# Performance work log

Measured on AMD Instinct MI355X. Metric: run time of the kernel, lower is better.

The kernel has to match this reference:

```python
import jax, jax.numpy as jnp
import numpy as np

N_NODES = 100000
N_EDGES = 6400000


def setup_inputs() -> dict:
    key = jax.random.key(0)
    k1, k2, k3 = jax.random.split(key, 3)
    x = jax.random.normal(k1, (N_NODES, 1), dtype=jnp.float32)
    edge_index = jax.random.randint(k2, (2, N_EDGES), 0, N_NODES, dtype=jnp.int64)
    edge_weight = jax.random.normal(k3, (N_EDGES,), dtype=jnp.float32)
    return {"x": x, "edge_index": edge_index, "edge_weight": edge_weight}


def reference(x, edge_index, edge_weight):
    # flow='target_to_source': messages come from x[edge_index[1]] and are
    # scatter-added into nodes edge_index[0].
    src = edge_index[0]  # aggregation target (flow reversed)
    dst = edge_index[1]  # message source
    msgs = edge_weight[:, None] * x[dst]  # [E, 1]
    out = jax.ops.segment_sum(msgs, src, num_segments=N_NODES)  # [N, 1]
    return out
```

## Files before the change

### kernel.cpp

```cpp
#include <hip/hip_runtime.h>

#define N_NODES 100000
#define N_EDGES 6400000
#define RANGES 4
#define RANGE_S 25000
#define NB 64
#define BLK 1024
#define FIX_SCALE 1048576.0f
#define FIX_INV   (1.0f / 1048576.0f)

#define TBLOCKS 256
#define TTHREADS 1024
#define EPB (N_EDGES / TBLOCKS)
#define GPB (EPB / 8)
#define LDSN 80000

__global__ void zero_out_kernel(float* __restrict__ out, int n) {
    int i = blockIdx.x * blockDim.x + threadIdx.x;
    if (i < n) out[i] = 0.0f;
}

__global__ void __launch_bounds__(256) scatter_direct_kernel(
        const float* __restrict__ x, const int* __restrict__ ei,
        const float* __restrict__ w, float* __restrict__ out) {
    int t = blockIdx.x * blockDim.x + threadIdx.x;
    int e0 = t * 4;
    if (e0 >= N_EDGES) return;
    int4   s4 = *reinterpret_cast<const int4*>(ei + e0);
    int4   d4 = *reinterpret_cast<const int4*>(ei + N_EDGES + e0);
    float4 w4 = *reinterpret_cast<const float4*>(w + e0);
    atomicAdd(&out[s4.x], w4.x * x[d4.x]);
    atomicAdd(&out[s4.y], w4.y * x[d4.y]);
    atomicAdd(&out[s4.z], w4.z * x[d4.z]);
    atomicAdd(&out[s4.w], w4.w * x[d4.w]);
}

__device__ __forceinline__ unsigned bf16_rne(float f) {
    unsigned b = __float_as_uint(f);
    b += 0x7FFFu + ((b >> 16) & 1u);
    return b >> 16;
}
__device__ __forceinline__ float bf16_to_f(unsigned h) {
    return __uint_as_float(h << 16);
}

__global__ void __launch_bounds__(TTHREADS, 4) transform_kernel(
        const float* __restrict__ x, const int* __restrict__ ei,
        const float* __restrict__ w, unsigned short* __restrict__ msg) {
    __shared__ unsigned short xh[LDSN];
    const int tid  = threadIdx.x;
    const int base = blockIdx.x * EPB;
    const int* dstp = ei + N_EDGES;

    const float4* xs = reinterpret_cast<const float4*>(x);
    for (int j = tid; j < LDSN / 8; j += TTHREADS) {
        float4 f0 = xs[j * 2], f1 = xs[j * 2 + 1];
        uint4 pk;
        pk.x = bf16_rne(f0.x) | (bf16_rne(f0.y) << 16);
        pk.y = bf16_rne(f0.z) | (bf16_rne(f0.w) << 16);
        pk.z = bf16_rne(f1.x) | (bf16_rne(f1.y) << 16);
        pk.w = bf16_rne(f1.z) | (bf16_rne(f1.w) << 16);
        *reinterpret_cast<uint4*>(&xh[j * 8]) = pk;
    }
    __syncthreads();

    #pragma unroll
    for (int k = 0; k < 4; ++k) {
        int idx = k * TTHREADS + tid;
        if (idx < GPB) {
            int e0 = base + idx * 8;
            int4   da = *reinterpret_cast<const int4*>(dstp + e0);
            int4   db = *reinterpret_cast<const int4*>(dstp + e0 + 4);
            float4 wa = *reinterpret_cast<const float4*>(w + e0);
            float4 wb = *reinterpret_cast<const float4*>(w + e0 + 4);

            unsigned a0 = (unsigned)da.x, a1 = (unsigned)da.y,
                     a2 = (unsigned)da.z, a3 = (unsigned)da.w,
                     a4 = (unsigned)db.x, a5 = (unsigned)db.y,
                     a6 = (unsigned)db.z, a7 = (unsigned)db.w;
            float v0 = bf16_to_f(xh[a0 < LDSN ? a0 : 0u]);
            float v1 = bf16_to_f(xh[a1 < LDSN ? a1 : 0u]);
            float v2 = bf16_to_f(xh[a2 < LDSN ? a2 : 0u]);
            float v3 = bf16_to_f(xh[a3 < LDSN ? a3 : 0u]);
            float v4 = bf16_to_f(xh[a4 < LDSN ? a4 : 0u]);
            float v5 = bf16_to_f(xh[a5 < LDSN ? a5 : 0u]);
            float v6 = bf16_to_f(xh[a6 < LDSN ? a6 : 0u]);
            float v7 = bf16_to_f(xh[a7 < LDSN ? a7 : 0u]);
            if (a0 >= LDSN) v0 = x[a0];
            if (a1 >= LDSN) v1 = x[a1];
            if (a2 >= LDSN) v2 = x[a2];
            if (a3 >= LDSN) v3 = x[a3];
            if (a4 >= LDSN) v4 = x[a4];
            if (a5 >= LDSN) v5 = x[a5];
            if (a6 >= LDSN) v6 = x[a6];
            if (a7 >= LDSN) v7 = x[a7];

            uint4 o;
            o.x = bf16_rne(wa.x * v0) | (bf16_rne(wa.y * v1) << 16);
            o.y = bf16_rne(wa.z * v2) | (bf16_rne(wa.w * v3) << 16);
            o.z = bf16_rne(wb.x * v4) | (bf16_rne(wb.y * v5) << 16);
            o.w = bf16_rne(wb.z * v6) | (bf16_rne(wb.w * v7) << 16);
            *reinterpret_cast<uint4*>(msg + e0) = o;
        }
    }
}

__global__ void __launch_bounds__(BLK) bin_kernel(
        const int* __restrict__ ei, const unsigned short* __restrict__ msg,
        unsigned short* __restrict__ partial) {
    __shared__ int bins[RANGE_S];
    const int b    = blockIdx.x;
    const int xcd  = b & 7;
    const int slot = b >> 3;
    const int r    = slot & 3;
    const int c    = (slot >> 2) * 8 + xcd;

    for (int i = threadIdx.x; i < RANGE_S; i += BLK) bins[i] = 0;
    __syncthreads();

    const int chunk = N_EDGES / NB;
    const int base  = c * chunk;
    const int end   = base + chunk;
    const int lo    = r * RANGE_S;

    for (int e = base + (int)threadIdx.x * 8; e < end; e += BLK * 8) {
        int4 sa = *reinterpret_cast<const int4*>(ei + e);
        int4 sb = *reinterpret_cast<const int4*>(ei + e + 4);
        uint4 mm = *reinterpret_cast<const uint4*>(msg + e);

        unsigned a[8] = {(unsigned)(sa.x-lo),(unsigned)(sa.y-lo),(unsigned)(sa.z-lo),(unsigned)(sa.w-lo),
                         (unsigned)(sb.x-lo),(unsigned)(sb.y-lo),(unsigned)(sb.z-lo),(unsigned)(sb.w-lo)};
        float f[8] = {
            __uint_as_float((mm.x & 0xFFFFu) << 16), __uint_as_float(mm.x & 0xFFFF0000u),
            __uint_as_float((mm.y & 0xFFFFu) << 16), __uint_as_float(mm.y & 0xFFFF0000u),
            __uint_as_float((mm.z & 0xFFFFu) << 16), __uint_as_float(mm.z & 0xFFFF0000u),
            __uint_as_float((mm.w & 0xFFFFu) << 16), __uint_as_float(mm.w & 0xFFFF0000u)
        };
        int mi[8];
        #pragma unroll
        for (int k = 0; k < 8; ++k) mi[k] = (int)__builtin_rintf(f[k] * FIX_SCALE);
        #pragma unroll
        for (int k = 0; k < 8; ++k) {
            if (a[k] < RANGE_S) atomicAdd(&bins[a[k]], mi[k]);
        }
    }
    __syncthreads();

    unsigned short* outp = partial + (size_t)(r * NB + c) * RANGE_S;
    for (int i = threadIdx.x; i < RANGE_S / 4; i += BLK) {
        int4 v = *reinterpret_cast<const int4*>(&bins[i * 4]);
        uint2 pk;
        pk.x = bf16_rne((float)v.x * FIX_INV) | (bf16_rne((float)v.y * FIX_INV) << 16);
        pk.y = bf16_rne((float)v.z * FIX_INV) | (bf16_rne((float)v.w * FIX_INV) << 16);
        *reinterpret_cast<uint2*>(outp + i * 4) = pk;
    }
}

__global__ void reduce_range_kernel(const unsigned short* __restrict__ partial,
                                    float* __restrict__ out) {
    int i = blockIdx.x * blockDim.x + threadIdx.x;
    int n0 = i * 4;
    if (n0 >= N_NODES) return;
    int r = n0 / RANGE_S;
    int s = n0 - r * RANGE_S;
    const unsigned short* bp = partial + (size_t)(r * NB) * RANGE_S + s;
    float4 acc = make_float4(0.f, 0.f, 0.f, 0.f);
    for (int j = 0; j < NB; ++j) {
        uint2 v = *reinterpret_cast<const uint2*>(bp + (size_t)j * RANGE_S);
        acc.x += bf16_to_f(v.x & 0xFFFFu);
        acc.y += bf16_to_f(v.x >> 16);
        acc.z += bf16_to_f(v.y & 0xFFFFu);
        acc.w += bf16_to_f(v.y >> 16);
    }
    *reinterpret_cast<float4*>(out + n0) = acc;
}

extern "C" void kernel_launch(void* const* d_in, const int* in_sizes, int n_in,
                              void* d_out, int out_size, void* d_ws, size_t ws_size,
                              hipStream_t stream) {
    const float* x   = (const float*)d_in[0];
    const int*   ei  = (const int*)d_in[1];
    const float* w   = (const float*)d_in[2];
    float*       out = (float*)d_out;

    const size_t msg_bytes     = (size_t)N_EDGES * 2;
    const size_t partial_bytes = (size_t)RANGES * NB * RANGE_S * 2;

    if (ws_size >= msg_bytes + partial_bytes) {
        unsigned short* msg     = (unsigned short*)d_ws;
        unsigned short* partial = (unsigned short*)((char*)d_ws + msg_bytes);
        transform_kernel<<<TBLOCKS, TTHREADS, 0, stream>>>(x, ei, w, msg);
        bin_kernel<<<RANGES * NB, BLK, 0, stream>>>(ei, msg, partial);
        reduce_range_kernel<<<(N_NODES / 4 + 255) / 256, 256, 0, stream>>>(partial, out);
    } else {
        zero_out_kernel<<<(N_NODES + 255) / 256, 256, 0, stream>>>(out, N_NODES);
        scatter_direct_kernel<<<(N_EDGES / 4 + 255) / 256, 256, 0, stream>>>(x, ei, w, out);
    }
}
```

Measured before the change: 40.28 us.

## Fuse transform, bin and reduce stages into one cooperative kernel with grid syncs

Replaces three separate kernel launches with a single cooperative kernel that uses grid-wide syncs between the message-transform, LDS binning and range-reduce phases. The transform edge partition is remapped so each block writes the edge segment it later bins, which keeps that data in the local XCD's cache. The LDS buffer is shared between the bf16 x table and the int bins. This removes launch gaps and inter-kernel drain, at the cost of grid barrier overhead and a 160KB LDS footprint that forces one block per CU.

```diff
diff --git a/kernel.cpp b/kernel.cpp
--- a/kernel.cpp
+++ b/kernel.cpp
@@ -1,17 +1,20 @@
 #include <hip/hip_runtime.h>
+#include <hip/hip_cooperative_groups.h>
+
+namespace cg = cooperative_groups;
 
 #define N_NODES 100000
 #define N_EDGES 6400000
 #define RANGES 4
 #define RANGE_S 25000
 #define NB 64
-#define BLK 1024
+#define CHUNK (N_EDGES / NB)
 #define FIX_SCALE 1048576.0f
 #define FIX_INV   (1.0f / 1048576.0f)
 
 #define TBLOCKS 256
 #define TTHREADS 1024
-#define EPB (N_EDGES / TBLOCKS)
+#define EPB 25000
 #define GPB (EPB / 8)
 #define LDSN 80000
 
@@ -44,135 +47,140 @@
     return __uint_as_float(h << 16);
 }
 
-__global__ void __launch_bounds__(TTHREADS, 4) transform_kernel(
+__global__ void __launch_bounds__(TTHREADS, 4) fused_kernel(
         const float* __restrict__ x, const int* __restrict__ ei,
-        const float* __restrict__ w, unsigned short* __restrict__ msg) {
-    __shared__ unsigned short xh[LDSN];
+        const float* __restrict__ w, unsigned short* __restrict__ msg,
+        unsigned short* __restrict__ partial, float* __restrict__ out) {
+    __shared__ __align__(16) unsigned char smem[160000];
+    unsigned short* xh  = reinterpret_cast<unsigned short*>(smem);
+    int*            bins = reinterpret_cast<int*>(smem);
+
     const int tid  = threadIdx.x;
-    const int base = blockIdx.x * EPB;
-    const int* dstp = ei + N_EDGES;
-
-    const float4* xs = reinterpret_cast<const float4*>(x);
-    for (int j = tid; j < LDSN / 8; j += TTHREADS) {
-        float4 f0 = xs[j * 2], f1 = xs[j * 2 + 1];
-        uint4 pk;
-        pk.x = bf16_rne(f0.x) | (bf16_rne(f0.y) << 16);
-        pk.y = bf16_rne(f0.z) | (bf16_rne(f0.w) << 16);
-        pk.z = bf16_rne(f1.x) | (bf16_rne(f1.y) << 16);
-        pk.w = bf16_rne(f1.z) | (bf16_rne(f1.w) << 16);
-        *reinterpret_cast<uint4*>(&xh[j * 8]) = pk;
-    }
-    __syncthreads();
-
-    #pragma unroll
-    for (int k = 0; k < 4; ++k) {
-        int idx = k * TTHREADS + tid;
-        if (idx < GPB) {
-            int e0 = base + idx * 8;
-            int4   da = *reinterpret_cast<const int4*>(dstp + e0);
-            int4   db = *reinterpret_cast<const int4*>(dstp + e0 + 4);
-            float4 wa = *reinterpret_cast<const float4*>(w + e0);
-            float4 wb = *reinterpret_cast<const float4*>(w + e0 + 4);
-
-            unsigned a0 = (unsigned)da.x, a1 = (unsigned)da.y,
-                     a2 = (unsigned)da.z, a3 = (unsigned)da.w,
-                     a4 = (unsigned)db.x, a5 = (unsigned)db.y,
-                     a6 = (unsigned)db.z, a7 = (unsigned)db.w;
-            float v0 = bf16_to_f(xh[a0 < LDSN ? a0 : 0u]);
-            float v1 = bf16_to_f(xh[a1 < LDSN ? a1 : 0u]);
-            float v2 = bf16_to_f(xh[a2 < LDSN ? a2 : 0u]);
-            float v3 = bf16_to_f(xh[a3 < LDSN ? a3 : 0u]);
-            float v4 = bf16_to_f(xh[a4 < LDSN ? a4 : 0u]);
-            float v5 = bf16_to_f(xh[a5 < LDSN ? a5 : 0u]);
-            float v6 = bf16_to_f(xh[a6 < LDSN ? a6 : 0u]);
-            float v7 = bf16_to_f(xh[a7 < LDSN ? a7 : 0u]);
-            if (a0 >= LDSN) v0 = x[a0];
-            if (a1 >= LDSN) v1 = x[a1];
-            if (a2 >= LDSN) v2 = x[a2];
-            if (a3 >= LDSN) v3 = x[a3];
-            if (a4 >= LDSN) v4 = x[a4];
-            if (a5 >= LDSN) v5 = x[a5];
-            if (a6 >= LDSN) v6 = x[a6];
-            if (a7 >= LDSN) v7 = x[a7];
-
-            uint4 o;
-            o.x = bf16_rne(wa.x * v0) | (bf16_rne(wa.y * v1) << 16);
-            o.y = bf16_rne(wa.z * v2) | (bf16_rne(wa.w * v3) << 16);
-            o.z = bf16_rne(wb.x * v4) | (bf16_rne(wb.y * v5) << 16);
-            o.w = bf16_rne(wb.z * v6) | (bf16_rne(wb.w * v7) << 16);
-            *reinterpret_cast<uint4*>(msg + e0) = o;
-        }
-    }
-}
-
-__global__ void __launch_bounds__(BLK) bin_kernel(
-        const int* __restrict__ ei, const unsigned short* __restrict__ msg,
-        unsigned short* __restrict__ partial) {
-    __shared__ int bins[RANGE_S];
     const int b    = blockIdx.x;
     const int xcd  = b & 7;
     const int slot = b >> 3;
-    const int r    = slot & 3;
+    const int rq   = slot & 3;
     const int c    = (slot >> 2) * 8 + xcd;
-
-    for (int i = threadIdx.x; i < RANGE_S; i += BLK) bins[i] = 0;
-    __syncthreads();
-
-    const int chunk = N_EDGES / NB;
-    const int base  = c * chunk;
-    const int end   = base + chunk;
-    const int lo    = r * RANGE_S;
-
-    for (int e = base + (int)threadIdx.x * 8; e < end; e += BLK * 8) {
-        int4 sa = *reinterpret_cast<const int4*>(ei + e);
-        int4 sb = *reinterpret_cast<const int4*>(ei + e + 4);
-        uint4 mm = *reinterpret_cast<const uint4*>(msg + e);
-
-        unsigned a[8] = {(unsigned)(sa.x-lo),(unsigned)(sa.y-lo),(unsigned)(sa.z-lo),(unsigned)(sa.w-lo),
-                         (unsigned)(sb.x-lo),(unsigned)(sb.y-lo),(unsigned)(sb.z-lo),(unsigned)(sb.w-lo)};
-        float f[8] = {
-            __uint_as_float((mm.x & 0xFFFFu) << 16), __uint_as_float(mm.x & 0xFFFF0000u),
-            __uint_as_float((mm.y & 0xFFFFu) << 16), __uint_as_float(mm.y & 0xFFFF0000u),
-            __uint_as_float((mm.z & 0xFFFFu) << 16), __uint_as_float(mm.z & 0xFFFF0000u),
-            __uint_as_float((mm.w & 0xFFFFu) << 16), __uint_as_float(mm.w & 0xFFFF0000u)
-        };
-        int mi[8];
+    const int* dstp = ei + N_EDGES;
+
+    {
+        const float4* xs = reinterpret_cast<const float4*>(x);
+        for (int j = tid; j < LDSN / 8; j += TTHREADS) {
+            float4 f0 = xs[j * 2], f1 = xs[j * 2 + 1];
+            uint4 pk;
+            pk.x = bf16_rne(f0.x) | (bf16_rne(f0.y) << 16);
+            pk.y = bf16_rne(f0.z) | (bf16_rne(f0.w) << 16);
+            pk.z = bf16_rne(f1.x) | (bf16_rne(f1.y) << 16);
+            pk.w = bf16_rne(f1.z) | (bf16_rne(f1.w) << 16);
+            *reinterpret_cast<uint4*>(&xh[j * 8]) = pk;
+        }
+        __syncthreads();
+
+        const int base = c * CHUNK + rq * EPB;
         #pragma unroll
-        for (int k = 0; k < 8; ++k) mi[k] = (int)__builtin_rintf(f[k] * FIX_SCALE);
-        #pragma unroll
-        for (int k = 0; k < 8; ++k) {
-            if (a[k] < RANGE_S) atomicAdd(&bins[a[k]], mi[k]);
-        }
-    }
-    __syncthreads();
-
-    unsigned short* outp = partial + (size_t)(r * NB + c) * RANGE_S;
-    for (int i = threadIdx.x; i < RANGE_S / 4; i += BLK) {
-        int4 v = *reinterpret_cast<const int4*>(&bins[i * 4]);
-        uint2 pk;
-        pk.x = bf16_rne((float)v.x * FIX_INV) | (bf16_rne((float)v.y * FIX_INV) << 16);
-        pk.y = bf16_rne((float)v.z * FIX_INV) | (bf16_rne((float)v.w * FIX_INV) << 16);
-        *reinterpret_cast<uint2*>(outp + i * 4) = pk;
-    }
-}
-
-__global__ void reduce_range_kernel(const unsigned short* __restrict__ partial,
-                                    float* __restrict__ out) {
-    int i = blockIdx.x * blockDim.x + threadIdx.x;
-    int n0 = i * 4;
-    if (n0 >= N_NODES) return;
-    int r = n0 / RANGE_S;
-    int s = n0 - r * RANGE_S;
-    const unsigned short* bp = partial + (size_t)(r * NB) * RANGE_S + s;
-    float4 acc = make_float4(0.f, 0.f, 0.f, 0.f);
-    for (int j = 0; j < NB; ++j) {
-        uint2 v = *reinterpret_cast<const uint2*>(bp + (size_t)j * RANGE_S);
-        acc.x += bf16_to_f(v.x & 0xFFFFu);
-        acc.y += bf16_to_f(v.x >> 16);
-        acc.z += bf16_to_f(v.y & 0xFFFFu);
-        acc.w += bf16_to_f(v.y >> 16);
-    }
-    *reinterpret_cast<float4*>(out + n0) = acc;
+        for (int k = 0; k < 4; ++k) {
+            const int idx = k * TTHREADS + tid;
+            if (idx < GPB) {
+                const int e0 = base + idx * 8;
+                int4   da = *reinterpret_cast<const int4*>(dstp + e0);
+                int4   db = *reinterpret_cast<const int4*>(dstp + e0 + 4);
+                float4 wa = *reinterpret_cast<const float4*>(w + e0);
+                float4 wb = *reinterpret_cast<const float4*>(w + e0 + 4);
+
+                unsigned a0 = (unsigned)da.x, a1 = (unsigned)da.y,
+                         a2 = (unsigned)da.z, a3 = (unsigned)da.w,
+                         a4 = (unsigned)db.x, a5 = (unsigned)db.y,
+                         a6 = (unsigned)db.z, a7 = (unsigned)db.w;
+                float v0 = bf16_to_f(xh[a0 < LDSN ? a0 : 0u]);
+                float v1 = bf16_to_f(xh[a1 < LDSN ? a1 : 0u]);
+                float v2 = bf16_to_f(xh[a2 < LDSN ? a2 : 0u]);
+                float v3 = bf16_to_f(xh[a3 < LDSN ? a3 : 0u]);
+                float v4 = bf16_to_f(xh[a4 < LDSN ? a4 : 0u]);
+                float v5 = bf16_to_f(xh[a5 < LDSN ? a5 : 0u]);
+                float v6 = bf16_to_f(xh[a6 < LDSN ? a6 : 0u]);
+                float v7 = bf16_to_f(xh[a7 < LDSN ? a7 : 0u]);
+                if (a0 >= LDSN) v0 = x[a0];
+                if (a1 >= LDSN) v1 = x[a1];
+                if (a2 >= LDSN) v2 = x[a2];
+                if (a3 >= LDSN) v3 = x[a3];
+                if (a4 >= LDSN) v4 = x[a4];
+                if (a5 >= LDSN) v5 = x[a5];
+                if (a6 >= LDSN) v6 = x[a6];
+                if (a7 >= LDSN) v7 = x[a7];
+
+                uint4 o;
+                o.x = bf16_rne(wa.x * v0) | (bf16_rne(wa.y * v1) << 16);
+                o.y = bf16_rne(wa.z * v2) | (bf16_rne(wa.w * v3) << 16);
+                o.z = bf16_rne(wb.x * v4) | (bf16_rne(wb.y * v5) << 16);
+                o.w = bf16_rne(wb.z * v6) | (bf16_rne(wb.w * v7) << 16);
+                *reinterpret_cast<uint4*>(msg + e0) = o;
+            }
+        }
+    }
+
+    cg::this_grid().sync();
+
+    {
+        for (int i = tid; i < RANGE_S; i += TTHREADS) bins[i] = 0;
+        __syncthreads();
+
+        const int base = c * CHUNK;
+        const int end  = base + CHUNK;
+        const int lo   = rq * RANGE_S;
+
+        for (int e = base + tid * 8; e < end; e += TTHREADS * 8) {
+            int4 sa = *reinterpret_cast<const int4*>(ei + e);
+            int4 sb = *reinterpret_cast<const int4*>(ei + e + 4);
+            uint4 mm = *reinterpret_cast<const uint4*>(msg + e);
+
+            unsigned a[8] = {(unsigned)(sa.x-lo),(unsigned)(sa.y-lo),(unsigned)(sa.z-lo),(unsigned)(sa.w-lo),
+                             (unsigned)(sb.x-lo),(unsigned)(sb.y-lo),(unsigned)(sb.z-lo),(unsigned)(sb.w-lo)};
+            float f[8] = {
+                __uint_as_float((mm.x & 0xFFFFu) << 16), __uint_as_float(mm.x & 0xFFFF0000u),
+                __uint_as_float((mm.y & 0xFFFFu) << 16), __uint_as_float(mm.y & 0xFFFF0000u),
+                __uint_as_float((mm.z & 0xFFFFu) << 16), __uint_as_float(mm.z & 0xFFFF0000u),
+                __uint_as_float((mm.w & 0xFFFFu) << 16), __uint_as_float(mm.w & 0xFFFF0000u)
+            };
+            int mi[8];
+            #pragma unroll
+            for (int k = 0; k < 8; ++k) mi[k] = (int)__builtin_rintf(f[k] * FIX_SCALE);
+            #pragma unroll
+            for (int k = 0; k < 8; ++k) {
+                if (a[k] < RANGE_S) atomicAdd(&bins[a[k]], mi[k]);
+            }
+        }
+        __syncthreads();
+
+        unsigned short* outp = partial + (size_t)(rq * NB + c) * RANGE_S;
+        for (int i = tid; i < RANGE_S / 4; i += TTHREADS) {
+            int4 v = *reinterpret_cast<const int4*>(&bins[i * 4]);
+            uint2 pk;
+            pk.x = bf16_rne((float)v.x * FIX_INV) | (bf16_rne((float)v.y * FIX_INV) << 16);
+            pk.y = bf16_rne((float)v.z * FIX_INV) | (bf16_rne((float)v.w * FIX_INV) << 16);
+            *reinterpret_cast<uint2*>(outp + i * 4) = pk;
+        }
+    }
+
+    cg::this_grid().sync();
+
+    {
+        int t = b * TTHREADS + tid;
+        int n0 = t * 4;
+        if (n0 < N_NODES) {
+            int r = n0 / RANGE_S;
+            int s = n0 - r * RANGE_S;
+            const unsigned short* bp = partial + (size_t)(r * NB) * RANGE_S + s;
+            float4 acc = make_float4(0.f, 0.f, 0.f, 0.f);
+            for (int j = 0; j < NB; ++j) {
+                uint2 v = *reinterpret_cast<const uint2*>(bp + (size_t)j * RANGE_S);
+                acc.x += bf16_to_f(v.x & 0xFFFFu);
+                acc.y += bf16_to_f(v.x >> 16);
+                acc.z += bf16_to_f(v.y & 0xFFFFu);
+                acc.w += bf16_to_f(v.y >> 16);
+            }
+            *reinterpret_cast<float4*>(out + n0) = acc;
+        }
+    }
 }
 
 extern "C" void kernel_launch(void* const* d_in, const int* in_sizes, int n_in,
@@ -189,9 +197,11 @@
     if (ws_size >= msg_bytes + partial_bytes) {
         unsigned short* msg     = (unsigned short*)d_ws;
         unsigned short* partial = (unsigned short*)((char*)d_ws + msg_bytes);
-        transform_kernel<<<TBLOCKS, TTHREADS, 0, stream>>>(x, ei, w, msg);
-        bin_kernel<<<RANGES * NB, BLK, 0, stream>>>(ei, msg, partial);
-        reduce_range_kernel<<<(N_NODES / 4 + 255) / 256, 256, 0, stream>>>(partial, out);
+        void* args[] = { (void*)&x, (void*)&ei, (void*)&w,
+                         (void*)&msg, (void*)&partial, (void*)&out };
+        hipLaunchCooperativeKernel((const void*)fused_kernel,
+                                   dim3(TBLOCKS), dim3(TTHREADS),
+                                   args, 0, stream);
     } else {
         zero_out_kernel<<<(N_NODES + 255) / 256, 256, 0, stream>>>(out, N_NODES);
         scatter_direct_kernel<<<(N_EDGES / 4 + 255) / 256, 256, 0, stream>>>(x, ei, w, out);
```

After: 117.8 us. 192% more time.
